# Performance work log

Hardware: AMD Instinct MI355X
Metric: run time of the kernel (lower is better)

The kernel has to match this reference:

```python
import jax, jax.numpy as jnp
import numpy as np
from jax import lax

# Model dims (see init_kwargs / mamba_ssm defaults)
B_, L_, D_IN = 8, 512, 128
D_MODEL, N_LAYERS = 512, 2
EXPAND, D_STATE, D_CONV = 2, 16, 4
D_INNER = EXPAND * D_MODEL          # 1024
DT_RANK = (D_MODEL + 15) // 16      # 32


def setup_inputs() -> dict:
    key = jax.random.key(0)
    ks = iter(jax.random.split(key, 32))
    def p(shape, scale=0.02):
        return jax.random.normal(next(ks), shape, jnp.float32) * scale
    inp = {}
    inp["x"] = jax.random.normal(next(ks), (B_, L_, D_IN), jnp.float32)
    # input projection (Linear(input_dim, d_model), with bias)
    inp["proj_in_w"] = p((D_MODEL, D_IN))
    inp["proj_in_b"] = p((D_MODEL,))
    # stacked per-layer Mamba params (leading dim = N_LAYERS)
    inp["in_proj_w"] = p((N_LAYERS, 2 * D_INNER, D_MODEL))      # no bias (mamba default)
    inp["conv_w"]    = p((N_LAYERS, D_INNER, D_CONV))           # depthwise conv1d
    inp["conv_b"]    = p((N_LAYERS, D_INNER))
    inp["x_proj_w"]  = p((N_LAYERS, DT_RANK + 2 * D_STATE, D_INNER))
    inp["dt_proj_w"] = p((N_LAYERS, D_INNER, DT_RANK))
    inp["dt_proj_b"] = jnp.full((N_LAYERS, D_INNER), 0.1, jnp.float32)
    inp["A_log"]     = jnp.log(jnp.tile(jnp.arange(1, D_STATE + 1, dtype=jnp.float32), (N_LAYERS, D_INNER, 1)))
    inp["Dm"]        = jnp.ones((N_LAYERS, D_INNER), jnp.float32)
    inp["out_proj_w"] = p((N_LAYERS, D_MODEL, D_INNER))         # no bias
    # classifier head: Linear(d_model, 64) -> ReLU -> Linear(64, 1)
    inp["cls_w1"] = p((64, D_MODEL)); inp["cls_b1"] = p((64,))
    inp["cls_w2"] = p((1, 64));       inp["cls_b2"] = p((1,))
    return inp


def _mamba_block(h, in_w, cw, cb, xp_w, dt_w, dt_b, A_log, Dm, out_w):
    B, L, _ = h.shape
    xz = jnp.einsum('bld,ed->ble', h, in_w)           # (B, L, 2*d_inner)
    xi, z = jnp.split(xz, 2, axis=-1)
    # causal depthwise conv1d (pad left d_conv-1, crop to L)
    xc = xi.transpose(0, 2, 1)                         # (B, d_inner, L)
    xc = lax.conv_general_dilated(
        xc, cw[:, None, :], (1,), [(D_CONV - 1, 0)],
        feature_group_count=D_INNER,
        dimension_numbers=('NCH', 'OIH', 'NCH')) + cb[None, :, None]
    xc = jax.nn.silu(xc).transpose(0, 2, 1)            # (B, L, d_inner)
    x_dbl = jnp.einsum('bld,ed->ble', xc, xp_w)        # (B, L, dt_rank + 2*d_state)
    dt, Bm, Cm = jnp.split(x_dbl, [DT_RANK, DT_RANK + D_STATE], axis=-1)
    dt = jax.nn.softplus(jnp.einsum('blr,dr->bld', dt, dt_w) + dt_b)  # (B, L, d_inner)
    A = -jnp.exp(A_log)                                # (d_inner, d_state)

    def step(hst, ins):
        dt_t, B_t, C_t, x_t = ins                      # (B,di),(B,ds),(B,ds),(B,di)
        dA = jnp.exp(dt_t[..., None] * A)              # (B, di, ds)
        hst = dA * hst + (dt_t * x_t)[..., None] * B_t[:, None, :]
        y = jnp.einsum('bds,bs->bd', hst, C_t)
        return hst, y

    h0 = jnp.zeros((B, D_INNER, D_STATE), h.dtype)
    xs = (dt.transpose(1, 0, 2), Bm.transpose(1, 0, 2),
          Cm.transpose(1, 0, 2), xc.transpose(1, 0, 2))
    _, ys = lax.scan(step, h0, xs)                     # ys: (L, B, d_inner)
    y = ys.transpose(1, 0, 2) + xc * Dm                # skip term D*x
    y = y * jax.nn.silu(z)                             # gate
    return jnp.einsum('ble,de->bld', y, out_w)         # (B, L, d_model)


def reference(x, proj_in_w, proj_in_b, in_proj_w, conv_w, conv_b, x_proj_w,
              dt_proj_w, dt_proj_b, A_log, Dm, out_proj_w,
              cls_w1, cls_b1, cls_w2, cls_b2):
    h = jnp.einsum('bli,di->bld', x, proj_in_w) + proj_in_b
    for l in range(N_LAYERS):
        h = _mamba_block(h, in_proj_w[l], conv_w[l], conv_b[l], x_proj_w[l],
                         dt_proj_w[l], dt_proj_b[l], A_log[l], Dm[l], out_proj_w[l])
    h = h.mean(axis=1)                                 # (B, d_model); dropout = identity (eval)
    h = jax.nn.relu(h @ cls_w1.T + cls_b1)
    logits = (h @ cls_w2.T + cls_b2).squeeze(-1)       # (B,)
    return logits
```

## Files before the change

kernel.cpp:

```cpp
#include <hip/hip_runtime.h>
#include <hip/hip_bf16.h>

#define B_   8
#define L_   512
#define DIN  128
#define DM   512
#define NLAY 2
#define DI   1024
#define DS   16
#define DTR  32
#define BL   (B_ * L_)
#define KS   8
#define CL   128
#define NCH  (L_ / CL)

typedef short bf16x8 __attribute__((ext_vector_type(8)));
typedef float floatx4 __attribute__((ext_vector_type(4)));

__device__ __forceinline__ unsigned short f2bf(float f) {
    unsigned int u = __float_as_uint(f);
    unsigned int r = (u + 0x7FFF + ((u >> 16) & 1)) >> 16;
    return (unsigned short)r;
}
__device__ __forceinline__ float bf2f(unsigned short u) {
    return __uint_as_float((unsigned int)u << 16);
}

#if __has_builtin(__builtin_amdgcn_exp2f)
#define EXP2(x) __builtin_amdgcn_exp2f(x)
#else
#define EXP2(x) __expf((x) * 0.69314718056f)
#endif

__device__ __forceinline__ void gld_lds16(const unsigned short* g, unsigned short* l) {
    __builtin_amdgcn_global_load_lds(
        (const __attribute__((address_space(1))) void*)g,
        (__attribute__((address_space(3))) void*)l,
        16, 0, 0);
}

__device__ __forceinline__ bf16x8 ldcvt_bf8(const float* __restrict__ p) {
    float4 a = *(const float4*)p;
    float4 b = *(const float4*)(p + 4);
    unsigned short o[8];
    o[0] = f2bf(a.x); o[1] = f2bf(a.y); o[2] = f2bf(a.z); o[3] = f2bf(a.w);
    o[4] = f2bf(b.x); o[5] = f2bf(b.y); o[6] = f2bf(b.z); o[7] = f2bf(b.w);
    return *(bf16x8*)o;
}

__global__ __launch_bounds__(256) void cvt_all(
    const float* __restrict__ x,  unsigned short* __restrict__ xbf,
    const float* __restrict__ pw, unsigned short* __restrict__ wpin,
    const float* __restrict__ iw, unsigned short* __restrict__ win,
    const float* __restrict__ ow, unsigned short* __restrict__ wout,
    const float* __restrict__ dtp, unsigned short* __restrict__ dtwb,
    float* __restrict__ hm)
{
    int bid = blockIdx.x;
    if (bid >= 1856) {
        int i = (bid - 1856) * 2048 + threadIdx.x * 8;
        float4 z = make_float4(0.f, 0.f, 0.f, 0.f);
        *(float4*)(hm + i) = z;
        *(float4*)(hm + i + 4) = z;
        return;
    }
    const float* src; unsigned short* dst; int off;
    if      (bid < 256)  { src = x;   dst = xbf;  off = bid; }
    else if (bid < 288)  { src = pw;  dst = wpin; off = bid - 256; }
    else if (bid < 1312) { src = iw;  dst = win;  off = bid - 288; }
    else if (bid < 1824) { src = ow;  dst = wout; off = bid - 1312; }
    else                 { src = dtp; dst = dtwb; off = bid - 1824; }
    int i = (off * 256 + threadIdx.x) * 8;
    float4 a = *(const float4*)(src + i);
    float4 b = *(const float4*)(src + i + 4);
    unsigned short o[8];
    o[0] = f2bf(a.x); o[1] = f2bf(a.y); o[2] = f2bf(a.z); o[3] = f2bf(a.w);
    o[4] = f2bf(b.x); o[5] = f2bf(b.y); o[6] = f2bf(b.z); o[7] = f2bf(b.w);
    *(uint4*)(dst + i) = *(uint4*)o;
}

__global__ __launch_bounds__(256) void gemm_mfma(
    const unsigned short* __restrict__ A,
    const unsigned short* __restrict__ W,
    float* __restrict__ C, unsigned short* __restrict__ Cb,
    int N, int K)
{
    __shared__ unsigned short As[128 * 64];
    __shared__ unsigned short Ws[128 * 64];

    const int tid  = threadIdx.x;
    const int lane = tid & 63;
    const int wv   = tid >> 6;
    const int wm   = (wv >> 1) * 64;
    const int wn   = (wv & 1) * 64;
    const int lr   = lane & 15;
    const int q    = lane >> 4;

    const int srow  = lane >> 3;
    const int skcol = (lane & 7) * 8;
    const long aRowBase = (long)blockIdx.y * 128;
    const long wRowBase = (long)blockIdx.x * 128;

    floatx4 acc[4][4];
#pragma unroll
    for (int i = 0; i < 4; ++i)
#pragma unroll
        for (int j = 0; j < 4; ++j)
#pragma unroll
            for (int r = 0; r < 4; ++r) acc[i][j][r] = 0.f;

    for (int k0 = 0; k0 < K; k0 += 64) {
        __syncthreads();
#pragma unroll
        for (int c = 0; c < 4; ++c) {
            const int chunk = wv * 4 + c;
            const int row   = chunk * 8 + srow;
            gld_lds16(A + (aRowBase + row) * K + k0 + skcol,
                      As + chunk * 512 + lane * 8);
            gld_lds16(W + (wRowBase + row) * K + k0 + skcol,
                      Ws + chunk * 512 + lane * 8);
        }
        __syncthreads();

#pragma unroll
        for (int kk = 0; kk < 2; ++kk) {
            bf16x8 af[4], bfr[4];
#pragma unroll
            for (int i = 0; i < 4; ++i)
                af[i] = *(const bf16x8*)(As + (wm + i * 16 + lr) * 64 + kk * 32 + q * 8);
#pragma unroll
            for (int j = 0; j < 4; ++j)
                bfr[j] = *(const bf16x8*)(Ws + (wn + j * 16 + lr) * 64 + kk * 32 + q * 8);
#pragma unroll
            for (int i = 0; i < 4; ++i)
#pragma unroll
                for (int j = 0; j < 4; ++j)
                    acc[i][j] = __builtin_amdgcn_mfma_f32_16x16x32_bf16(
                        af[i], bfr[j], acc[i][j], 0, 0, 0);
        }
    }

#pragma unroll
    for (int i = 0; i < 4; ++i) {
#pragma unroll
        for (int r = 0; r < 4; ++r) {
            const int  crow = blockIdx.y * 128 + wm + i * 16 + q * 4 + r;
            const long base = (long)crow * N + blockIdx.x * 128 + wn + lr;
#pragma unroll
            for (int j = 0; j < 4; ++j) {
                float v = acc[i][j][r];
                if (C)  C[base + j * 16] = v;
                if (Cb) Cb[base + j * 16] = f2bf(v);
            }
        }
    }
}

__global__ __launch_bounds__(256) void gemm_mfma_n64(
    const unsigned short* __restrict__ A,
    const unsigned short* __restrict__ W,
    const float* __restrict__ bias,
    float* __restrict__ C, unsigned short* __restrict__ Cb,
    int N, int K, int meanmode, float* __restrict__ hm)
{
    __shared__ unsigned short As[128 * 64];
    __shared__ unsigned short Ws[64 * 64];
    __shared__ float colsum[64];

    const int tid  = threadIdx.x;
    const int lane = tid & 63;
    const int wv   = tid >> 6;
    const int wm   = wv * 32;
    const int lr   = lane & 15;
    const int q    = lane >> 4;

    const int srow  = lane >> 3;
    const int skcol = (lane & 7) * 8;
    const long aRowBase = (long)blockIdx.y * 128;
    const long wRowBase = (long)blockIdx.x * 64;

    floatx4 acc[2][4];
#pragma unroll
    for (int i = 0; i < 2; ++i)
#pragma unroll
        for (int j = 0; j < 4; ++j)
#pragma unroll
            for (int r = 0; r < 4; ++r) acc[i][j][r] = 0.f;

    for (int k0 = 0; k0 < K; k0 += 64) {
        __syncthreads();
#pragma unroll
        for (int c = 0; c < 4; ++c) {
            const int chunk = wv * 4 + c;
            const int row   = chunk * 8 + srow;
            gld_lds16(A + (aRowBase + row) * K + k0 + skcol,
                      As + chunk * 512 + lane * 8);
        }
#pragma unroll
        for (int c = 0; c < 2; ++c) {
            const int chunk = wv * 2 + c;
            const int row   = chunk * 8 + srow;
            gld_lds16(W + (wRowBase + row) * K + k0 + skcol,
                      Ws + chunk * 512 + lane * 8);
        }
        __syncthreads();

#pragma unroll
        for (int kk = 0; kk < 2; ++kk) {
            bf16x8 af[2], bfr[4];
#pragma unroll
            for (int i = 0; i < 2; ++i)
                af[i] = *(const bf16x8*)(As + (wm + i * 16 + lr) * 64 + kk * 32 + q * 8);
#pragma unroll
            for (int j = 0; j < 4; ++j)
                bfr[j] = *(const bf16x8*)(Ws + (j * 16 + lr) * 64 + kk * 32 + q * 8);
#pragma unroll
            for (int i = 0; i < 2; ++i)
#pragma unroll
                for (int j = 0; j < 4; ++j)
                    acc[i][j] = __builtin_amdgcn_mfma_f32_16x16x32_bf16(
                        af[i], bfr[j], acc[i][j], 0, 0, 0);
        }
    }

    if (meanmode) {
        if (tid < 64) colsum[tid] = 0.f;
        __syncthreads();
#pragma unroll
        for (int j = 0; j < 4; ++j) {
            float p = 0.f;
#pragma unroll
            for (int i = 0; i < 2; ++i)
#pragma unroll
                for (int r = 0; r < 4; ++r) p += acc[i][j][r];
            atomicAdd(&colsum[j * 16 + lr], p);
        }
        __syncthreads();
        if (tid < 64) {
            const int b = blockIdx.y >> 2;
            atomicAdd(&hm[b * DM + blockIdx.x * 64 + tid],
                      colsum[tid] * (1.f / (float)L_));
        }
        return;
    }

    float bj[4] = {0.f, 0.f, 0.f, 0.f};
    if (bias) {
#pragma unroll
        for (int j = 0; j < 4; ++j)
            bj[j] = bias[blockIdx.x * 64 + j * 16 + lr];
    }
#pragma unroll
    for (int i = 0; i < 2; ++i) {
#pragma unroll
        for (int r = 0; r < 4; ++r) {
            const int  crow = blockIdx.y * 128 + wm + i * 16 + q * 4 + r;
            const long base = (long)crow * N + blockIdx.x * 64 + lr;
#pragma unroll
            for (int j = 0; j < 4; ++j) {
                float v = acc[i][j][r] + bj[j];
                if (C)  C[base + j * 16] = v;
                if (Cb) Cb[base + j * 16] = f2bf(v);
            }
        }
    }
}

__global__ __launch_bounds__(256) void xprojconv(
    const unsigned short* __restrict__ xzb, const float* __restrict__ cw,
    const float* __restrict__ cb, const float* __restrict__ W,
    float* __restrict__ P, float* __restrict__ xcout)
{
    __shared__ float As[16][68];
    __shared__ float Ws[16][68];

    const int tid  = threadIdx.x;
    const int tx   = tid & 15;
    const int ty   = tid >> 4;
    const int lrow = tid >> 2;
    const int lk   = (tid & 3) << 2;
    const int kbase = blockIdx.x * (DI / KS);

    const int m = blockIdx.y * 64 + lrow;
    const int t = m & (L_ - 1);
    const float* Wp = W + lrow * DI + kbase + lk;

    float acc[4][4] = {};

    for (int k0 = 0; k0 < DI / KS; k0 += 16) {
        const int dcol = kbase + k0 + lk;
        float4 cbv = *(const float4*)(cb + dcol);
        float sums[4] = {cbv.x, cbv.y, cbv.z, cbv.w};
        float4 cwq[4];
#pragma unroll
        for (int q = 0; q < 4; ++q) cwq[q] = *(const float4*)(cw + (dcol + q) * 4);
#pragma unroll
        for (int w = 0; w < 4; ++w) {
            int tw = t - 3 + w;
            if (tw >= 0) {
                const uint2 up = *(const uint2*)(xzb + (long)(m - 3 + w) * (2 * DI) + dcol);
                float x0 = __uint_as_float(up.x << 16);
                float x1 = __uint_as_float(up.x & 0xffff0000u);
                float x2 = __uint_as_float(up.y << 16);
                float x3 = __uint_as_float(up.y & 0xffff0000u);
                sums[0] += ((const float*)&cwq[0])[w] * x0;
                sums[1] += ((const float*)&cwq[1])[w] * x1;
                sums[2] += ((const float*)&cwq[2])[w] * x2;
                sums[3] += ((const float*)&cwq[3])[w] * x3;
            }
        }
        float4 a4;
#pragma unroll
        for (int q = 0; q < 4; ++q)
            ((float*)&a4)[q] = sums[q] / (1.f + __expf(-sums[q]));
        float4 wv = *(const float4*)(Wp + k0);
        *(float4*)(xcout + (long)(dcol >> 4) * (BL * 16) + (long)m * 16 + lk) = a4;

        __syncthreads();
        As[lk + 0][lrow] = a4.x; As[lk + 1][lrow] = a4.y;
        As[lk + 2][lrow] = a4.z; As[lk + 3][lrow] = a4.w;
        Ws[lk + 0][lrow] = wv.x; Ws[lk + 1][lrow] = wv.y;
        Ws[lk + 2][lrow] = wv.z; Ws[lk + 3][lrow] = wv.w;
        __syncthreads();
#pragma unroll
        for (int k = 0; k < 16; ++k) {
            const float4 a44 = *(const float4*)&As[k][ty << 2];
            const float4 w4  = *(const float4*)&Ws[k][tx << 2];
            acc[0][0] += a44.x * w4.x; acc[0][1] += a44.x * w4.y;
            acc[0][2] += a44.x * w4.z; acc[0][3] += a44.x * w4.w;
            acc[1][0] += a44.y * w4.x; acc[1][1] += a44.y * w4.y;
            acc[1][2] += a44.y * w4.z; acc[1][3] += a44.y * w4.w;
            acc[2][0] += a44.z * w4.x; acc[2][1] += a44.z * w4.y;
            acc[2][2] += a44.z * w4.z; acc[2][3] += a44.z * w4.w;
            acc[3][0] += a44.w * w4.x; acc[3][1] += a44.w * w4.y;
            acc[3][2] += a44.w * w4.z; acc[3][3] += a44.w * w4.w;
        }
    }

    float* out = P + (long)blockIdx.x * (BL * 64)
               + (blockIdx.y * 64 + (ty << 2)) * 64 + (tx << 2);
#pragma unroll
    for (int i = 0; i < 4; ++i)
        *(float4*)(out + i * 64) = make_float4(acc[i][0], acc[i][1],
                                               acc[i][2], acc[i][3]);
}

__global__ __launch_bounds__(256) void xproj_reduce(
    const float* __restrict__ P, float* __restrict__ xdbl)
{
    int i = (blockIdx.x * 256 + threadIdx.x) * 4;
    float4 s = *(const float4*)(P + i);
#pragma unroll
    for (int k = 1; k < KS; ++k) {
        float4 p = *(const float4*)(P + (long)k * (BL * 64) + i);
        s.x += p.x; s.y += p.y; s.z += p.z; s.w += p.w;
    }
    *(float4*)(xdbl + i) = s;
}

template <int CTRL>
__device__ __forceinline__ float dpp_shr_add(float v) {
    int sh = __builtin_amdgcn_update_dpp(0, __float_as_int(v), CTRL, 0xF, 0xF, true);
    return v + __int_as_float(sh);
}

__global__ __launch_bounds__(256) void scan_fused(
    const float* __restrict__ xc, const float* __restrict__ xdbl,
    const unsigned short* __restrict__ dtwb,
    const float* __restrict__ dtpb,
    const float* __restrict__ A_log, const float* __restrict__ Dm,
    const unsigned short* __restrict__ xzb, unsigned short* __restrict__ ysb16)
{
    __shared__ float4 sdp [CL / 2][17];
    __shared__ float4 sbc4[CL / 2][17];
    __shared__ float  sy  [16][CL + 4];

    const int tid  = threadIdx.x;
    const int s    = tid & 15;
    const int grp  = tid >> 4;
    const int bd0  = blockIdx.x * 16;
    const int b    = bd0 >> 10;
    const int d0   = bd0 & (DI - 1);
    const int mb0  = b * L_;

    const int j    = tid & 15;
    const int tt   = tid >> 4;
    const int lane = tid & 63;
    const int w    = tid >> 6;
    const int q    = lane >> 4;
    const int tW   = 32 * w;

    const float a    = -__expf(A_log[(d0 + grp) * DS + s]);
    const float dmv  = Dm[d0 + j];
    const float bias = dtpb[d0 + j];

    const float* xcc = xc + (long)(d0 >> 4) * (BL * 16);

    const bf16x8 bfrag = *(const bf16x8*)(dtwb + (d0 + j) * 32 + q * 8);

    float  rB[8], rC[8];
    bf16x8 ra[2];
    float  rxc[2][4], rz[2][4];

#pragma unroll
    for (int i = 0; i < 8; ++i) {
        int m = mb0 + tt + 16 * i;
        rB[i] = xdbl[m * 64 + DTR + j];
        rC[i] = xdbl[m * 64 + DTR + DS + j];
    }
#pragma unroll
    for (int tile = 0; tile < 2; ++tile) {
        ra[tile] = ldcvt_bf8(xdbl + (long)(mb0 + tW + tile * 16 + j) * 64 + q * 8);
#pragma unroll
        for (int r = 0; r < 4; ++r) {
            int t = tW + tile * 16 + q * 4 + r;
            rxc[tile][r] = xcc[(long)(mb0 + t) * 16 + j];
            rz [tile][r] = bf2f(xzb[(long)(mb0 + t) * (2 * DI) + DI + d0 + j]);
        }
    }

    float state = 0.f;

    for (int c = 0; c < NCH; ++c) {
        const int mbase = mb0 + c * CL;
        float xcur[2][4], zcur[2][4];
#pragma unroll
        for (int tile = 0; tile < 2; ++tile)
#pragma unroll
            for (int r = 0; r < 4; ++r) {
                xcur[tile][r] = rxc[tile][r];
                zcur[tile][r] = rz[tile][r];
            }

        floatx4 dacc[2];
#pragma unroll
        for (int tile = 0; tile < 2; ++tile) {
            floatx4 cin;
            cin[0] = bias; cin[1] = bias; cin[2] = bias; cin[3] = bias;
            dacc[tile] = __builtin_amdgcn_mfma_f32_16x16x32_bf16(
                ra[tile], bfrag, cin, 0, 0, 0);
        }

        __syncthreads();
#pragma unroll
        for (int i = 0; i < 8; ++i) {
            int t = tt + 16 * i;
            ((float2*)&sbc4[t >> 1][j])[t & 1] = make_float2(rB[i], rC[i]);
        }
#pragma unroll
        for (int tile = 0; tile < 2; ++tile) {
#pragma unroll
            for (int r = 0; r < 4; ++r) {
                int t = tW + tile * 16 + q * 4 + r;
                float v = dacc[tile][r];
                float dt = (v > 20.f) ? v : __logf(1.f + __expf(v));
                ((float2*)&sdp[t >> 1][j])[t & 1] =
                    make_float2(dt * 1.44269504f, dt * xcur[tile][r]);
            }
        }
        __syncthreads();

        if (c < NCH - 1) {
            const int mn = mbase + CL;
#pragma unroll
            for (int i = 0; i < 8; ++i) {
                int m = mn + tt + 16 * i;
                rB[i] = xdbl[m * 64 + DTR + j];
                rC[i] = xdbl[m * 64 + DTR + DS + j];
            }
#pragma unroll
            for (int tile = 0; tile < 2; ++tile) {
                ra[tile] = ldcvt_bf8(xdbl + (long)(mn + tW + tile * 16 + j) * 64 + q * 8);
#pragma unroll
                for (int r = 0; r < 4; ++r) {
                    int t = tW + tile * 16 + q * 4 + r;
                    rxc[tile][r] = xcc[(long)(mn + t) * 16 + j];
                    rz [tile][r] = bf2f(xzb[(long)(mn + t) * (2 * DI) + DI + d0 + j]);
                }
            }
        }

        float4 dp0 = sdp[0][grp], bc0 = sbc4[0][s];
        float4 dp1 = sdp[1][grp], bc1 = sbc4[1][s];
        for (int t4 = 0; t4 < CL; t4 += 4) {
            const int t2n = (t4 >> 1) + 2;
            const int t2c = (t2n < CL / 2) ? t2n : 0;
            float4 dpn0 = sdp[t2c][grp];
            float4 bcn0 = sbc4[t2c][s];
            float4 dpn1 = sdp[t2c + 1][grp];
            float4 bcn1 = sbc4[t2c + 1][s];

            float ybuf[4];
            {
                const float dA = EXP2(dp0.x * a);
                state = fmaf(dA, state, dp0.y * bc0.x);
                float contrib = state * bc0.y;
                contrib = dpp_shr_add<0x111>(contrib);
                contrib = dpp_shr_add<0x112>(contrib);
                contrib = dpp_shr_add<0x114>(contrib);
                contrib = dpp_shr_add<0x118>(contrib);
                ybuf[0] = contrib;
            }
            {
                const float dA = EXP2(dp0.z * a);
                state = fmaf(dA, state, dp0.w * bc0.z);
                float contrib = state * bc0.w;
                contrib = dpp_shr_add<0x111>(contrib);
                contrib = dpp_shr_add<0x112>(contrib);
                contrib = dpp_shr_add<0x114>(contrib);
                contrib = dpp_shr_add<0x118>(contrib);
                ybuf[1] = contrib;
            }
            {
                const float dA = EXP2(dp1.x * a);
                state = fmaf(dA, state, dp1.y * bc1.x);
                float contrib = state * bc1.y;
                contrib = dpp_shr_add<0x111>(contrib);
                contrib = dpp_shr_add<0x112>(contrib);
                contrib = dpp_shr_add<0x114>(contrib);
                contrib = dpp_shr_add<0x118>(contrib);
                ybuf[2] = contrib;
            }
            {
                const float dA = EXP2(dp1.z * a);
                state = fmaf(dA, state, dp1.w * bc1.z);
                float contrib = state * bc1.w;
                contrib = dpp_shr_add<0x111>(contrib);
                contrib = dpp_shr_add<0x112>(contrib);
                contrib = dpp_shr_add<0x114>(contrib);
                contrib = dpp_shr_add<0x118>(contrib);
                ybuf[3] = contrib;
            }
            if (s == 15) *(float4*)&sy[grp][t4] = *(float4*)ybuf;
            dp0 = dpn0; bc0 = bcn0; dp1 = dpn1; bc1 = bcn1;
        }
        __syncthreads();

#pragma unroll
        for (int tile = 0; tile < 2; ++tile) {
#pragma unroll
            for (int r = 0; r < 4; ++r) {
                int t = tW + tile * 16 + q * 4 + r;
                float z = zcur[tile][r];
                float sz = z / (1.f + __expf(-z));
                float val = (sy[j][t] + xcur[tile][r] * dmv) * sz;
                ysb16[(long)(mbase + t) * DI + d0 + j] = f2bf(val);
            }
        }
    }
}

__global__ __launch_bounds__(512) void meancls_kernel(
    const float* __restrict__ hm, const float* __restrict__ w1,
    const float* __restrict__ b1, const float* __restrict__ w2,
    const float* __restrict__ b2, float* __restrict__ out)
{
    __shared__ float shm[DM];
    __shared__ float su[64];
    const int b = blockIdx.x, tid = threadIdx.x;
    shm[tid] = hm[b * DM + tid];
    __syncthreads();

    const int j = tid >> 3, sl = tid & 7;
    const float* wr = w1 + j * DM + sl * 64;
    const float* hb = shm + sl * 64;
    float p = 0.f;
    for (int k = 0; k < 64; k += 4)
        p += hb[k] * wr[k] + hb[k+1] * wr[k+1]
           + hb[k+2] * wr[k+2] + hb[k+3] * wr[k+3];
    p += __shfl_xor(p, 1);
    p += __shfl_xor(p, 2);
    p += __shfl_xor(p, 4);
    if (sl == 0) su[j] = fmaxf(p + b1[j], 0.f) * w2[j];
    __syncthreads();
    if (tid < 64) {
        float v = su[tid];
#pragma unroll
        for (int off = 32; off; off >>= 1) v += __shfl_down(v, off);
        if (tid == 0) out[b] = v + b2[0];
    }
}

extern "C" void kernel_launch(void* const* d_in, const int* in_sizes, int n_in,
                              void* d_out, int out_size, void* d_ws, size_t ws_size,
                              hipStream_t stream) {
    const float* x          = (const float*)d_in[0];
    const float* proj_in_w  = (const float*)d_in[1];
    const float* proj_in_b  = (const float*)d_in[2];
    const float* in_proj_w  = (const float*)d_in[3];
    const float* conv_w     = (const float*)d_in[4];
    const float* conv_b     = (const float*)d_in[5];
    const float* x_proj_w   = (const float*)d_in[6];
    const float* dt_proj_w  = (const float*)d_in[7];
    const float* dt_proj_b  = (const float*)d_in[8];
    const float* A_log      = (const float*)d_in[9];
    const float* Dm         = (const float*)d_in[10];
    const float* out_proj_w = (const float*)d_in[11];
    const float* cls_w1     = (const float*)d_in[12];
    const float* cls_b1     = (const float*)d_in[13];
    const float* cls_w2     = (const float*)d_in[14];
    const float* cls_b2     = (const float*)d_in[15];
    float* out = (float*)d_out;

    float* ws   = (float*)d_ws;
    float* h    = ws;
    float* xzf  = h    + BL * DM;
    float* xcb  = xzf  + BL * 2 * DI;
    float* xdbl = xcb  + BL * DI;
    float* scr  = xdbl + BL * 64;
    float* hm   = scr  + 2 * BL * DI;
    float* hmp  = hm   + B_ * DM;
    unsigned short* xzb  = (unsigned short*)xzf;
    unsigned short* u16  = (unsigned short*)(hmp + 64 * DM);
    unsigned short* xbf  = u16;
    unsigned short* hbf  = xbf  + BL * DIN;
    unsigned short* ysbf = hbf  + BL * DM;
    unsigned short* wpin = ysbf + BL * DI;
    unsigned short* win  = wpin + DM * DIN;
    unsigned short* wout = win  + NLAY * 2 * DI * DM;

    float* xpart = scr;
    unsigned short* dtwb = (unsigned short*)(scr + 6 * 1024 * 1024 + 262144 + 131072 + 16384);

    cvt_all<<<1858, 256, 0, stream>>>(x, xbf, proj_in_w, wpin,
                                      in_proj_w, win, out_proj_w, wout,
                                      dt_proj_w, dtwb, hm);

    gemm_mfma_n64<<<dim3(DM / 64, BL / 128), 256, 0, stream>>>(
        xbf, wpin, proj_in_b, nullptr, hbf, DM, DIN, 0, nullptr);

    for (int l = 0; l < NLAY; ++l) {
        gemm_mfma<<<dim3(2 * DI / 128, BL / 128), 256, 0, stream>>>(
            hbf, win + l * 2 * DI * DM, nullptr, xzb, 2 * DI, DM);
        xprojconv<<<dim3(KS, 64), 256, 0, stream>>>(
            xzb, conv_w + l * DI * 4, conv_b + l * DI,
            x_proj_w + l * 64 * DI, xpart, xcb);
        xproj_reduce<<<256, 256, 0, stream>>>(xpart, xdbl);
        scan_fused<<<(B_ * DI) / 16, 256, 0, stream>>>(
            xcb, xdbl, dtwb + l * DI * 32, dt_proj_b + l * DI,
            A_log + l * DI * DS, Dm + l * DI, xzb, ysbf);
        if (l == NLAY - 1) {
            gemm_mfma_n64<<<dim3(DM / 64, BL / 128), 256, 0, stream>>>(
                ysbf, wout + l * DM * DI, nullptr, nullptr, nullptr,
                DM, DI, 1, hm);
        } else {
            gemm_mfma_n64<<<dim3(DM / 64, BL / 128), 256, 0, stream>>>(
                ysbf, wout + l * DM * DI, nullptr, nullptr, hbf,
                DM, DI, 0, nullptr);
        }
    }

    meancls_kernel<<<B_, 512, 0, stream>>>(hm, cls_w1, cls_b1,
                                           cls_w2, cls_b2, out);
}
```

Measured before the change: 307.8 us.

## Fuse split-K reduction and classifier head via last-block atomic counters

Result: slower. 401.2 us (+30.3%).

```diff
diff --git a/kernel.cpp b/kernel.cpp
--- a/kernel.cpp
+++ b/kernel.cpp
@@ -54,10 +54,12 @@
     const float* __restrict__ iw, unsigned short* __restrict__ win,
     const float* __restrict__ ow, unsigned short* __restrict__ wout,
     const float* __restrict__ dtp, unsigned short* __restrict__ dtwb,
-    float* __restrict__ hm)
+    float* __restrict__ hm, int* __restrict__ cnt)
 {
     int bid = blockIdx.x;
     if (bid >= 1856) {
+        if (bid == 1856 && threadIdx.x < 17)
+            ((int4*)cnt)[threadIdx.x] = make_int4(0, 0, 0, 0);
         int i = (bid - 1856) * 2048 + threadIdx.x * 8;
         float4 z = make_float4(0.f, 0.f, 0.f, 0.f);
         *(float4*)(hm + i) = z;
@@ -161,11 +163,16 @@
     const unsigned short* __restrict__ W,
     const float* __restrict__ bias,
     float* __restrict__ C, unsigned short* __restrict__ Cb,
-    int N, int K, int meanmode, float* __restrict__ hm)
+    int N, int K, int meanmode, float* __restrict__ hm,
+    const float* __restrict__ w1, const float* __restrict__ b1,
+    const float* __restrict__ w2, const float* __restrict__ b2,
+    float* __restrict__ out, int* __restrict__ cnt2)
 {
     __shared__ unsigned short As[128 * 64];
     __shared__ unsigned short Ws[64 * 64];
     __shared__ float colsum[64];
+    __shared__ float clsbuf[DM + 64];
+    __shared__ int lastFlag;
 
     const int tid  = threadIdx.x;
     const int lane = tid & 63;
@@ -241,6 +248,39 @@
             atomicAdd(&hm[b * DM + blockIdx.x * 64 + tid],
                       colsum[tid] * (1.f / (float)L_));
         }
+        __syncthreads();
+        if (tid == 0) {
+            __threadfence();
+            lastFlag = (atomicAdd(cnt2, 1) == 255);
+        }
+        __syncthreads();
+        if (lastFlag) {
+            __threadfence();
+            float* su = clsbuf + DM;
+            for (int b = 0; b < B_; ++b) {
+                clsbuf[tid]       = hm[b * DM + tid];
+                clsbuf[tid + 256] = hm[b * DM + tid + 256];
+                __syncthreads();
+                const int jj = tid >> 2, sl = tid & 3;
+                const float* wr = w1 + jj * DM + sl * 128;
+                const float* hb = clsbuf + sl * 128;
+                float p = 0.f;
+                for (int k = 0; k < 128; k += 4)
+                    p += hb[k] * wr[k] + hb[k+1] * wr[k+1]
+                       + hb[k+2] * wr[k+2] + hb[k+3] * wr[k+3];
+                p += __shfl_xor(p, 1);
+                p += __shfl_xor(p, 2);
+                if (sl == 0) su[jj] = fmaxf(p + b1[jj], 0.f) * w2[jj];
+                __syncthreads();
+                if (tid < 64) {
+                    float v = su[tid];
+#pragma unroll
+                    for (int off = 32; off; off >>= 1) v += __shfl_down(v, off);
+                    if (tid == 0) out[b] = v + b2[0];
+                }
+                __syncthreads();
+            }
+        }
         return;
     }
 
@@ -269,10 +309,12 @@
 __global__ __launch_bounds__(256) void xprojconv(
     const unsigned short* __restrict__ xzb, const float* __restrict__ cw,
     const float* __restrict__ cb, const float* __restrict__ W,
-    float* __restrict__ P, float* __restrict__ xcout)
+    float* __restrict__ P, float* __restrict__ xcout,
+    float* __restrict__ xdbl, int* __restrict__ cnt)
 {
     __shared__ float As[16][68];
     __shared__ float Ws[16][68];
+    __shared__ int lastFlag;
 
     const int tid  = threadIdx.x;
     const int tx   = tid & 15;
@@ -280,8 +322,9 @@
     const int lrow = tid >> 2;
     const int lk   = (tid & 3) << 2;
     const int kbase = blockIdx.x * (DI / KS);
-
-    const int m = blockIdx.y * 64 + lrow;
+    const int by   = blockIdx.y;
+
+    const int m = by * 64 + lrow;
     const int t = m & (L_ - 1);
     const float* Wp = W + lrow * DI + kbase + lk;
 
@@ -337,25 +380,36 @@
         }
     }
 
-    float* out = P + (long)blockIdx.x * (BL * 64)
-               + (blockIdx.y * 64 + (ty << 2)) * 64 + (tx << 2);
+    float* outp = P + (long)blockIdx.x * (BL * 64)
+                + (by * 64 + (ty << 2)) * 64 + (tx << 2);
 #pragma unroll
     for (int i = 0; i < 4; ++i)
-        *(float4*)(out + i * 64) = make_float4(acc[i][0], acc[i][1],
-                                               acc[i][2], acc[i][3]);
-}
-
-__global__ __launch_bounds__(256) void xproj_reduce(
-    const float* __restrict__ P, float* __restrict__ xdbl)
-{
-    int i = (blockIdx.x * 256 + threadIdx.x) * 4;
-    float4 s = *(const float4*)(P + i);
-#pragma unroll
-    for (int k = 1; k < KS; ++k) {
-        float4 p = *(const float4*)(P + (long)k * (BL * 64) + i);
-        s.x += p.x; s.y += p.y; s.z += p.z; s.w += p.w;
-    }
-    *(float4*)(xdbl + i) = s;
+        *(float4*)(outp + i * 64) = make_float4(acc[i][0], acc[i][1],
+                                                acc[i][2], acc[i][3]);
+
+    __syncthreads();
+    if (tid == 0) {
+        __threadfence();
+        int old = atomicAdd(&cnt[by], 1);
+        lastFlag = (old == KS - 1);
+        if (old == KS - 1) atomicExch(&cnt[by], 0);
+    }
+    __syncthreads();
+    if (lastFlag) {
+        __threadfence();
+        const int base = by * 4096 + tid * 16;
+#pragma unroll
+        for (int jj = 0; jj < 4; ++jj) {
+            const int idx = base + jj * 4;
+            float4 s = *(const float4*)(P + idx);
+#pragma unroll
+            for (int k = 1; k < KS; ++k) {
+                float4 p = *(const float4*)(P + (long)k * (BL * 64) + idx);
+                s.x += p.x; s.y += p.y; s.z += p.z; s.w += p.w;
+            }
+            *(float4*)(xdbl + idx) = s;
+        }
+    }
 }
 
 template <int CTRL>
@@ -395,7 +449,6 @@
     const float bias = dtpb[d0 + j];
 
     const float* xcc = xc + (long)(d0 >> 4) * (BL * 16);
-
     const bf16x8 bfrag = *(const bf16x8*)(dtwb + (d0 + j) * 32 + q * 8);
 
     float  rB[8], rC[8];
@@ -547,37 +600,6 @@
                 ysb16[(long)(mbase + t) * DI + d0 + j] = f2bf(val);
             }
         }
-    }
-}
-
-__global__ __launch_bounds__(512) void meancls_kernel(
-    const float* __restrict__ hm, const float* __restrict__ w1,
-    const float* __restrict__ b1, const float* __restrict__ w2,
-    const float* __restrict__ b2, float* __restrict__ out)
-{
-    __shared__ float shm[DM];
-    __shared__ float su[64];
-    const int b = blockIdx.x, tid = threadIdx.x;
-    shm[tid] = hm[b * DM + tid];
-    __syncthreads();
-
-    const int j = tid >> 3, sl = tid & 7;
-    const float* wr = w1 + j * DM + sl * 64;
-    const float* hb = shm + sl * 64;
-    float p = 0.f;
-    for (int k = 0; k < 64; k += 4)
-        p += hb[k] * wr[k] + hb[k+1] * wr[k+1]
-           + hb[k+2] * wr[k+2] + hb[k+3] * wr[k+3];
-    p += __shfl_xor(p, 1);
-    p += __shfl_xor(p, 2);
-    p += __shfl_xor(p, 4);
-    if (sl == 0) su[j] = fmaxf(p + b1[j], 0.f) * w2[j];
-    __syncthreads();
-    if (tid < 64) {
-        float v = su[tid];
-#pragma unroll
-        for (int off = 32; off; off >>= 1) v += __shfl_down(v, off);
-        if (tid == 0) out[b] = v + b2[0];
     }
 }
 
@@ -621,35 +643,35 @@
 
     float* xpart = scr;
     unsigned short* dtwb = (unsigned short*)(scr + 6 * 1024 * 1024 + 262144 + 131072 + 16384);
+    int* cnt  = (int*)hmp;
+    int* cnt2 = cnt + 64;
 
     cvt_all<<<1858, 256, 0, stream>>>(x, xbf, proj_in_w, wpin,
                                       in_proj_w, win, out_proj_w, wout,
-                                      dt_proj_w, dtwb, hm);
+                                      dt_proj_w, dtwb, hm, cnt);
 
     gemm_mfma_n64<<<dim3(DM / 64, BL / 128), 256, 0, stream>>>(
-        xbf, wpin, proj_in_b, nullptr, hbf, DM, DIN, 0, nullptr);
+        xbf, wpin, proj_in_b, nullptr, hbf, DM, DIN, 0, nullptr,
+        nullptr, nullptr, nullptr, nullptr, nullptr, nullptr);
 
     for (int l = 0; l < NLAY; ++l) {
         gemm_mfma<<<dim3(2 * DI / 128, BL / 128), 256, 0, stream>>>(
             hbf, win + l * 2 * DI * DM, nullptr, xzb, 2 * DI, DM);
         xprojconv<<<dim3(KS, 64), 256, 0, stream>>>(
             xzb, conv_w + l * DI * 4, conv_b + l * DI,
-            x_proj_w + l * 64 * DI, xpart, xcb);
-        xproj_reduce<<<256, 256, 0, stream>>>(xpart, xdbl);
+            x_proj_w + l * 64 * DI, xpart, xcb, xdbl, cnt);
         scan_fused<<<(B_ * DI) / 16, 256, 0, stream>>>(
             xcb, xdbl, dtwb + l * DI * 32, dt_proj_b + l * DI,
             A_log + l * DI * DS, Dm + l * DI, xzb, ysbf);
         if (l == NLAY - 1) {
             gemm_mfma_n64<<<dim3(DM / 64, BL / 128), 256, 0, stream>>>(
                 ysbf, wout + l * DM * DI, nullptr, nullptr, nullptr,
-                DM, DI, 1, hm);
+                DM, DI, 1, hm, cls_w1, cls_b1, cls_w2, cls_b2, out, cnt2);
         } else {
             gemm_mfma_n64<<<dim3(DM / 64, BL / 128), 256, 0, stream>>>(
                 ysbf, wout + l * DM * DI, nullptr, nullptr, hbf,
-                DM, DI, 0, nullptr);
-        }
-    }
-
-    meancls_kernel<<<B_, 512, 0, stream>>>(hm, cls_w1, cls_b1,
-                                           cls_w2, cls_b2, out);
-}
+                DM, DI, 0, nullptr,
+                nullptr, nullptr, nullptr, nullptr, nullptr, nullptr);
+        }
+    }
+}
```
